# Optimization experiments

Hardware: AMD Instinct MI355X
Metric: run time of the kernel (lower is better)

The kernel has to match this reference:

```python
import jax, jax.numpy as jnp
import numpy as np

D_MODEL = 1024
NUM_HEADS = 16
D_K = D_MODEL // NUM_HEADS


def setup_inputs() -> dict:
    key = jax.random.key(0)
    ks = jax.random.split(key, 5)
    s = 1.0 / np.sqrt(D_MODEL)
    return {
        "x": jax.random.normal(ks[0], (2, 2048, D_MODEL), dtype=jnp.float32),
        "Wq": jax.random.normal(ks[1], (D_MODEL, D_MODEL), dtype=jnp.float32) * s,
        "bq": jnp.zeros((D_MODEL,), jnp.float32),
        "Wk": jax.random.normal(ks[2], (D_MODEL, D_MODEL), dtype=jnp.float32) * s,
        "bk": jnp.zeros((D_MODEL,), jnp.float32),
        "Wv": jax.random.normal(ks[3], (D_MODEL, D_MODEL), dtype=jnp.float32) * s,
        "bv": jnp.zeros((D_MODEL,), jnp.float32),
        "Wo": jax.random.normal(ks[4], (D_MODEL, D_MODEL), dtype=jnp.float32) * s,
        "bo": jnp.zeros((D_MODEL,), jnp.float32),
    }


def reference(x, Wq, bq, Wk, bk, Wv, bv, Wo, bo):
    B, S, _ = x.shape

    def split_heads(t):  # [B,S,D] -> [B,H,S,d_k]
        return t.reshape(B, S, NUM_HEADS, D_K).transpose(0, 2, 1, 3)

    q = split_heads(x @ Wq + bq)
    k = split_heads(x @ Wk + bk)
    v = split_heads(x @ Wv + bv)

    # [B,H,S,S] scores, scaled by 1/sqrt(d_k)
    scores = jnp.einsum("bhqd,bhkd->bhqk", q, k) / jnp.sqrt(jnp.float32(D_K))
    causal = jnp.tril(jnp.ones((S, S), dtype=bool))  # True = keep
    scores = jnp.where(causal, scores, -jnp.inf)
    attn = jax.nn.softmax(scores, axis=-1)
    # dropout is identity in eval mode
    out = jnp.einsum("bhqk,bhkd->bhqd", attn, v)
    out = out.transpose(0, 2, 1, 3).reshape(B, S, D_MODEL)
    return out @ Wo + bo
```

## Files before the change

kernel.cpp:

```cpp
#include <hip/hip_runtime.h>
#include <stdint.h>

typedef __attribute__((ext_vector_type(8))) short bf16x8;
typedef __attribute__((ext_vector_type(8))) unsigned short ushort8;
typedef __attribute__((ext_vector_type(4))) float f32x4;
typedef __attribute__((ext_vector_type(16))) float f32x16;

constexpr int DM = 1024;
constexpr int SQ = 2048;
constexpr int NB = 2;
constexpr int NH = 16;
constexpr int DK = 64;
constexpr int M  = NB * SQ;

__device__ inline float bf2f(unsigned short u) {
    union { uint32_t i; float f; } c; c.i = ((uint32_t)u) << 16; return c.f;
}
__device__ inline unsigned short f2bf(float f) {
    union { float f; uint32_t i; } c; c.f = f;
    uint32_t r = c.i + 0x7FFFu + ((c.i >> 16) & 1u);
    return (unsigned short)(r >> 16);
}
__device__ inline float exp2v(float x) {
    float r;
    asm("v_exp_f32 %0, %1" : "=v"(r) : "v"(x));
    return r;
}
__device__ inline uint32_t cvtpk(float lo, float hi) {
    uint32_t r;
    asm("v_cvt_pk_bf16_f32 %0, %1, %2" : "=v"(r) : "v"(lo), "v"(hi));
    return r;
}
__device__ inline uint32_t sx32(uint32_t v) {
    return (uint32_t)__shfl_xor((int)v, 32);
}
__device__ inline float sx32f(float v) {
    return __shfl_xor(v, 32);
}
__device__ inline bf16x8 mkfrag(uint32_t a, uint32_t b, uint32_t c, uint32_t d) {
    union { bf16x8 v; uint32_t u[4]; } m;
    m.u[0] = a; m.u[1] = b; m.u[2] = c; m.u[3] = d;
    return m.v;
}
__device__ inline void gload_lds16(const unsigned short* g, unsigned short* l) {
    __builtin_amdgcn_global_load_lds(
        (const __attribute__((address_space(1))) void*)g,
        (__attribute__((address_space(3))) void*)l, 16, 0, 0);
}

__global__ __launch_bounds__(256) void cvt_x(const float* __restrict__ x,
                                             unsigned short* __restrict__ xb) {
    int idx = (blockIdx.x * 256 + threadIdx.x) * 8;
    const float* p = x + idx;
    ushort8 o;
#pragma unroll
    for (int i = 0; i < 8; ++i) o[i] = f2bf(p[i]);
    *(ushort8*)(xb + idx) = o;
}

__global__ __launch_bounds__(256) void cvt_w4(const float* __restrict__ W0,
                                              const float* __restrict__ W1,
                                              const float* __restrict__ W2,
                                              const float* __restrict__ W3,
                                              unsigned short* __restrict__ WtBase) {
    __shared__ float tile[32][33];
    const int z = blockIdx.z;
    const float* W = (z == 0) ? W0 : (z == 1) ? W1 : (z == 2) ? W2 : W3;
    unsigned short* Wt = WtBase + (size_t)z * DM * DM;
    int tx = threadIdx.x, ty = threadIdx.y;
    int bx = blockIdx.x, by = blockIdx.y;
#pragma unroll
    for (int j = 0; j < 4; ++j)
        tile[ty + j * 8][tx] = W[(size_t)(by * 32 + ty + j * 8) * DM + bx * 32 + tx];
    __syncthreads();
#pragma unroll
    for (int j = 0; j < 4; ++j)
        Wt[(size_t)(bx * 32 + ty + j * 8) * DM + by * 32 + tx] = f2bf(tile[tx][ty + j * 8]);
}

__global__ __launch_bounds__(256) void gemm128(const unsigned short* __restrict__ A,
                                               const unsigned short* __restrict__ Bt,
                                               const float* __restrict__ b0,
                                               const float* __restrict__ b1,
                                               const float* __restrict__ b2,
                                               unsigned short* __restrict__ outp) {
    constexpr int K = 1024;
    __shared__ __align__(16) unsigned short As[128 * 32];
    __shared__ __align__(16) unsigned short Bs[128 * 32];
    const int t = threadIdx.x;
    const int w = t >> 6, l = t & 63;
    const int l15 = l & 15, lg = l >> 4;
    const int wr = w >> 1, wc = w & 1;
    const int bx = blockIdx.x, by = blockIdx.y;

    f32x4 acc[4][4] = {};

    const int srow = l >> 2;
    const int sk   = (l & 3) * 8;
    const unsigned short* Abase = A  + (size_t)(by * 128) * K;
    const unsigned short* Bbase = Bt + (size_t)(bx * 128) * K;

    for (int k0 = 0; k0 < K; k0 += 32) {
#pragma unroll
        for (int i = 0; i < 2; ++i) {
            const int row = w * 32 + i * 16 + srow;
            gload_lds16(Abase + (size_t)row * K + k0 + sk, &As[row * 32 + sk]);
            gload_lds16(Bbase + (size_t)row * K + k0 + sk, &Bs[row * 32 + sk]);
        }
        __syncthreads();

        bf16x8 af[4], bfr[4];
#pragma unroll
        for (int mi = 0; mi < 4; ++mi)
            af[mi] = *(const bf16x8*)&As[(wr * 64 + mi * 16 + l15) * 32 + lg * 8];
#pragma unroll
        for (int ni = 0; ni < 4; ++ni)
            bfr[ni] = *(const bf16x8*)&Bs[(wc * 64 + ni * 16 + l15) * 32 + lg * 8];
#pragma unroll
        for (int mi = 0; mi < 4; ++mi)
#pragma unroll
            for (int ni = 0; ni < 4; ++ni)
                acc[mi][ni] = __builtin_amdgcn_mfma_f32_16x16x32_bf16(af[mi], bfr[ni], acc[mi][ni], 0, 0, 0);
        __syncthreads();
    }

#pragma unroll
    for (int ni = 0; ni < 4; ++ni) {
        const int n = bx * 128 + wc * 64 + ni * 16 + l15;
        const int mat = n >> 10;
        const float* bp = (mat == 0) ? b0 : (mat == 1) ? b1 : b2;
        const float bias = bp[n & 1023];
#pragma unroll
        for (int mi = 0; mi < 4; ++mi)
#pragma unroll
            for (int i = 0; i < 4; ++i) {
                const int m = by * 128 + wr * 64 + mi * 16 + lg * 4 + i;
                float v = acc[mi][ni][i] + bias;
                const int c = n & 1023;
                if (mat == 0) v *= 0.18033688f;
                const int h = c >> 6, d = c & 63;
                const int b = m >> 11, si = m & 2047;
                size_t idx;
                if (mat == 2)
                    idx = ((size_t)(b * NH + h) * DK + d) * SQ + si;
                else
                    idx = ((size_t)(b * NH + h) * SQ + si) * DK + d;
                outp[(size_t)mat * (NB * NH * SQ * DK) + idx] = f2bf(v);
            }
    }
}

__global__ __launch_bounds__(256) void gemm_wo(const unsigned short* __restrict__ A,
                                               const unsigned short* __restrict__ Bt,
                                               const float* __restrict__ bias,
                                               float* __restrict__ outp) {
    constexpr int K = 1024;
    __shared__ __align__(16) unsigned short As[128 * 32];
    __shared__ __align__(16) unsigned short Bs[64 * 32];
    const int t = threadIdx.x;
    const int w = t >> 6, l = t & 63;
    const int l15 = l & 15, lg = l >> 4;
    const int bx = blockIdx.x, by = blockIdx.y;

    f32x4 acc[2][4] = {};

    const int srow = l >> 2;
    const int sk   = (l & 3) * 8;
    const int brow = t >> 2;
    const int bk   = (t & 3) * 8;
    const unsigned short* Abase = A  + (size_t)(by * 128) * K;
    const unsigned short* Bbase = Bt + (size_t)(bx * 64) * K;

    for (int k0 = 0; k0 < K; k0 += 32) {
#pragma unroll
        for (int i = 0; i < 2; ++i) {
            const int row = w * 32 + i * 16 + srow;
            gload_lds16(Abase + (size_t)row * K + k0 + sk, &As[row * 32 + sk]);
        }
        gload_lds16(Bbase + (size_t)brow * K + k0 + bk, &Bs[brow * 32 + bk]);
        __syncthreads();

        bf16x8 af[2], bfr[4];
#pragma unroll
        for (int mi = 0; mi < 2; ++mi)
            af[mi] = *(const bf16x8*)&As[(w * 32 + mi * 16 + l15) * 32 + lg * 8];
#pragma unroll
        for (int ni = 0; ni < 4; ++ni)
            bfr[ni] = *(const bf16x8*)&Bs[(ni * 16 + l15) * 32 + lg * 8];
#pragma unroll
        for (int mi = 0; mi < 2; ++mi)
#pragma unroll
            for (int ni = 0; ni < 4; ++ni)
                acc[mi][ni] = __builtin_amdgcn_mfma_f32_16x16x32_bf16(af[mi], bfr[ni], acc[mi][ni], 0, 0, 0);
        __syncthreads();
    }

#pragma unroll
    for (int ni = 0; ni < 4; ++ni) {
        const int n = bx * 64 + ni * 16 + l15;
        const float bv = bias[n];
#pragma unroll
        for (int mi = 0; mi < 2; ++mi)
#pragma unroll
            for (int i = 0; i < 4; ++i) {
                const int m = by * 128 + w * 32 + mi * 16 + lg * 4 + i;
                outp[(size_t)m * DM + n] = acc[mi][ni][i] + bv;
            }
    }
}

__global__ __launch_bounds__(128) void attn32(const unsigned short* __restrict__ Qg,
                                              const unsigned short* __restrict__ Kg,
                                              const unsigned short* __restrict__ Vtg,
                                              unsigned short* __restrict__ O) {
    __shared__ __align__(16) char KV[2][16384];
    const float NEG_INF = -__builtin_inff();

    const int bid = blockIdx.x;
    const int bh  = bid & 31;
    const int qi  = 63 - (bid >> 5);
    const int b = bh >> 4, h = bh & 15;
    const size_t base = (size_t)bh * SQ * DK;

    const int t = threadIdx.x;
    const int w = t >> 6, l = t & 63;
    const int l31 = l & 31, hi = l >> 5;
    const bool h0 = (hi == 0);

    char* Ks0 = KV[w];
    char* Vs0 = KV[w] + 8192;
    float* myP = (float*)KV[w];
    float* otP = (float*)KV[w ^ 1];

    const int lrow = l >> 3;
    const int lchunk = (l & 7) ^ lrow;
    const unsigned short* ksrc0 = Kg + base + (size_t)lrow * DK + lchunk * 8;
    const unsigned short* vsrc0 = Vtg + (size_t)(bh * 64 + lrow) * SQ + lchunk * 8;

    int roff[4];
#pragma unroll
    for (int c = 0; c < 4; ++c) roff[c] = (hi * 16 + 32 * c) ^ ((l & 7) << 4);
    const int rb0 = l31 * 128, rb1 = (32 + l31) * 128;

    const int T    = (qi >> 1) + 1;
    const int Tmax = (T + 1) >> 1;
    const int qrow = qi * 32 + l31;

    bf16x8 qf[4];
    {
        const unsigned short* qp = Qg + base + (size_t)qrow * DK + hi * 8;
#pragma unroll
        for (int c = 0; c < 4; ++c) qf[c] = *(const bf16x8*)(qp + 16 * c);
    }

    float mrun = NEG_INF, lsum = 0.f;
    f32x16 o0 = {}, o1 = {};

#pragma unroll 1
    for (int i = 0; i < Tmax; ++i) {
        const int kt = 2 * i + w;
        const bool act = kt < T;
        if (act) {
            const unsigned short* ks = ksrc0 + (size_t)kt * 64 * DK;
            const unsigned short* vs = vsrc0 + kt * 64;
#pragma unroll
            for (int j = 0; j < 8; ++j)
                gload_lds16(ks + j * 8 * DK, (unsigned short*)Ks0 + j * 512 + l * 8);
#pragma unroll
            for (int j = 0; j < 8; ++j)
                gload_lds16(vs + (size_t)j * 8 * SQ, (unsigned short*)Vs0 + j * 512 + l * 8);
        }
        __syncthreads();
        if (!act) continue;

        f32x16 s0v = {}, s1v = {};
#pragma unroll
        for (int c = 0; c < 4; ++c) {
            bf16x8 ka0 = *(const bf16x8*)(Ks0 + rb0 + roff[c]);
            bf16x8 ka1 = *(const bf16x8*)(Ks0 + rb1 + roff[c]);
            s0v = __builtin_amdgcn_mfma_f32_32x32x16_bf16(ka0, qf[c], s0v, 0, 0, 0);
            s1v = __builtin_amdgcn_mfma_f32_32x32x16_bf16(ka1, qf[c], s1v, 0, 0, 0);
        }

        float s[32];
#pragma unroll
        for (int r = 0; r < 16; ++r) { s[r] = s0v[r]; s[16 + r] = s1v[r]; }
        if (kt == T - 1) {
            const int qrel = qrow - kt * 64;
#pragma unroll
            for (int r = 0; r < 16; ++r) {
                const int key0 = (r & 3) + 8 * (r >> 2) + 4 * hi;
                if (key0 > qrel) s[r] = NEG_INF;
                if (key0 + 32 > qrel) s[16 + r] = NEG_INF;
            }
        }

        float t8[8];
#pragma unroll
        for (int j = 0; j < 8; ++j)
            t8[j] = fmaxf(fmaxf(s[j], s[j + 8]), fmaxf(s[j + 16], s[j + 24]));
        float tm = fmaxf(fmaxf(fmaxf(t8[0], t8[1]), fmaxf(t8[2], t8[3])),
                         fmaxf(fmaxf(t8[4], t8[5]), fmaxf(t8[6], t8[7])));
        tm = fmaxf(tm, sx32f(tm));

        const float mn = fmaxf(mrun, tm);
        if (!__all(tm - mrun <= 11.0f)) {
            const float corr = exp2v(mrun - mn);
            lsum *= corr;
#pragma unroll
            for (int r = 0; r < 16; ++r) { o0[r] *= corr; o1[r] *= corr; }
            mrun = mn;
        }

#pragma unroll
        for (int r = 0; r < 32; ++r) s[r] = exp2v(s[r] - mrun);
        float a8[8];
#pragma unroll
        for (int j = 0; j < 8; ++j)
            a8[j] = (s[j] + s[j + 8]) + (s[j + 16] + s[j + 24]);
        lsum += ((a8[0] + a8[1]) + (a8[2] + a8[3])) + ((a8[4] + a8[5]) + (a8[6] + a8[7]));

        uint32_t pk[16];
#pragma unroll
        for (int j = 0; j < 16; ++j) pk[j] = cvtpk(s[2 * j], s[2 * j + 1]);
        const uint32_t X1 = sx32(h0 ? pk[2]  : pk[0]);
        const uint32_t X2 = sx32(h0 ? pk[3]  : pk[1]);
        const uint32_t X3 = sx32(h0 ? pk[6]  : pk[4]);
        const uint32_t X4 = sx32(h0 ? pk[7]  : pk[5]);
        const uint32_t X5 = sx32(h0 ? pk[10] : pk[8]);
        const uint32_t X6 = sx32(h0 ? pk[11] : pk[9]);
        const uint32_t X7 = sx32(h0 ? pk[14] : pk[12]);
        const uint32_t X8 = sx32(h0 ? pk[15] : pk[13]);
        bf16x8 pf[4];
        pf[0] = mkfrag(h0 ? pk[0]  : X1, h0 ? pk[1]  : X2, h0 ? X1 : pk[2],  h0 ? X2 : pk[3]);
        pf[1] = mkfrag(h0 ? pk[4]  : X3, h0 ? pk[5]  : X4, h0 ? X3 : pk[6],  h0 ? X4 : pk[7]);
        pf[2] = mkfrag(h0 ? pk[8]  : X5, h0 ? pk[9]  : X6, h0 ? X5 : pk[10], h0 ? X6 : pk[11]);
        pf[3] = mkfrag(h0 ? pk[12] : X7, h0 ? pk[13] : X8, h0 ? X7 : pk[14], h0 ? X8 : pk[15]);

#pragma unroll
        for (int vi = 0; vi < 4; ++vi) {
            bf16x8 va0 = *(const bf16x8*)(Vs0 + rb0 + roff[vi]);
            bf16x8 va1 = *(const bf16x8*)(Vs0 + rb1 + roff[vi]);
            o0 = __builtin_amdgcn_mfma_f32_32x32x16_bf16(va0, pf[vi], o0, 0, 0, 0);
            o1 = __builtin_amdgcn_mfma_f32_32x32x16_bf16(va1, pf[vi], o1, 0, 0, 0);
        }
    }

    lsum += sx32f(lsum);
    {
        float* pb = myP + (size_t)l * 40;
#pragma unroll
        for (int r = 0; r < 16; ++r) { pb[r] = o0[r]; pb[16 + r] = o1[r]; }
        pb[32] = mrun; pb[33] = lsum;
    }
    __syncthreads();
    {
        const float* qb = otP + (size_t)l * 40;
        const float pm = qb[32], pl = qb[33];
        const float mm = fmaxf(mrun, pm);
        const float ca = exp2v(mrun - mm);
        const float cb = exp2v(pm - mm);
        const float lm = lsum * ca + pl * cb;
        if (w == 0) {
            const float inv = 1.f / lm;
            unsigned short* op = O + ((size_t)(b * SQ + qrow)) * DM + h * 64;
#pragma unroll
            for (int r = 0; r < 16; r += 2) {
                const int d = (r & 3) + 8 * (r >> 2) + 4 * hi;
                const float e0 = o0[r] * ca + qb[r] * cb;
                const float e1 = o0[r + 1] * ca + qb[r + 1] * cb;
                const float f0 = o1[r] * ca + qb[16 + r] * cb;
                const float f1 = o1[r + 1] * ca + qb[16 + r + 1] * cb;
                uint32_t w0 = (uint32_t)f2bf(e0 * inv) | ((uint32_t)f2bf(e1 * inv) << 16);
                uint32_t w1 = (uint32_t)f2bf(f0 * inv) | ((uint32_t)f2bf(f1 * inv) << 16);
                *(uint32_t*)(op + d) = w0;
                *(uint32_t*)(op + 32 + d) = w1;
            }
        }
    }
}

extern "C" void kernel_launch(void* const* d_in, const int* in_sizes, int n_in,
                              void* d_out, int out_size, void* d_ws, size_t ws_size,
                              hipStream_t stream) {
    const float* x  = (const float*)d_in[0];
    const float* Wq = (const float*)d_in[1];
    const float* bq = (const float*)d_in[2];
    const float* Wk = (const float*)d_in[3];
    const float* bk = (const float*)d_in[4];
    const float* Wv = (const float*)d_in[5];
    const float* bv = (const float*)d_in[6];
    const float* Wo = (const float*)d_in[7];
    const float* bo = (const float*)d_in[8];
    float* out = (float*)d_out;

    char* ws = (char*)d_ws;
    const size_t XB_BYTES = (size_t)M * DM * 2;
    const size_t W_BYTES  = (size_t)DM * DM * 2;
    const size_t H_BYTES  = (size_t)NB * NH * SQ * DK * 2;
    unsigned short* xb  = (unsigned short*)ws;
    unsigned short* wqt = (unsigned short*)(ws + XB_BYTES);
    unsigned short* wot = (unsigned short*)(ws + XB_BYTES + 3 * W_BYTES);
    unsigned short* Qb  = (unsigned short*)(ws + XB_BYTES + 4 * W_BYTES);
    unsigned short* Kb  = (unsigned short*)(ws + XB_BYTES + 4 * W_BYTES + H_BYTES);
    unsigned short* Vb  = (unsigned short*)(ws + XB_BYTES + 4 * W_BYTES + 2 * H_BYTES);

    cvt_x<<<(M * DM) / (256 * 8), 256, 0, stream>>>(x, xb);
    cvt_w4<<<dim3(32, 32, 4), dim3(32, 8), 0, stream>>>(Wq, Wk, Wv, Wo, wqt);

    gemm128<<<dim3(24, 32), 256, 0, stream>>>(xb, wqt, bq, bk, bv, Qb);

    attn32<<<NB * NH * 64, 128, 0, stream>>>(Qb, Kb, Vb, xb );

    gemm_wo<<<dim3(16, 32), 256, 0, stream>>>(xb, wot, bo, out);
}
```

Baseline: 120.4 us.

## Restructure attention: two waves share K/V tiles with double-buffered LDS prefetch

Previously each block handled 32 query rows, and its two waves split the key tiles and merged partial softmax results at the end. Now each block covers 64 query rows (one 32-row slab per wave), and both waves consume the same cooperatively loaded K/V tile from LDS. That halves K/V global traffic per query and removes the cross-wave softmax merge. Loading is double-buffered, so the next tile is issued before computing on the current one. Blocks are ordered to interleave short and long causal rows for load balance. The trade-off is half as many blocks, and the wave for the even slab does masked work on the diagonal tile.

```diff
diff --git a/kernel.cpp b/kernel.cpp
--- a/kernel.cpp
+++ b/kernel.cpp
@@ -213,12 +213,18 @@
                                               const unsigned short* __restrict__ Kg,
                                               const unsigned short* __restrict__ Vtg,
                                               unsigned short* __restrict__ O) {
-    __shared__ __align__(16) char KV[2][16384];
+    __shared__ __align__(16) char BufA[16384];
+    __shared__ __align__(16) char BufB[16384];
     const float NEG_INF = -__builtin_inff();
 
     const int bid = blockIdx.x;
     const int bh  = bid & 31;
-    const int qi  = 63 - (bid >> 5);
+    const int g   = bid >> 5;
+    const int u = g & 7, gq = g >> 3;
+    const int j_even = 2 * u + (gq >> 1);
+    const int j_odd  = 31 - 2 * u - (gq >> 1);
+    const int j = (gq & 1) ? j_odd : j_even;
+
     const int b = bh >> 4, h = bh & 15;
     const size_t base = (size_t)bh * SQ * DK;
 
@@ -227,23 +233,19 @@
     const int l31 = l & 31, hi = l >> 5;
     const bool h0 = (hi == 0);
 
-    char* Ks0 = KV[w];
-    char* Vs0 = KV[w] + 8192;
-    float* myP = (float*)KV[w];
-    float* otP = (float*)KV[w ^ 1];
-
-    const int lrow = l >> 3;
-    const int lchunk = (l & 7) ^ lrow;
-    const unsigned short* ksrc0 = Kg + base + (size_t)lrow * DK + lchunk * 8;
-    const unsigned short* vsrc0 = Vtg + (size_t)(bh * 64 + lrow) * SQ + lchunk * 8;
+    const int trow = t >> 3;
+    const int tchunk = (t & 7) ^ (trow & 7);
+    const unsigned short* ksrc0 = Kg + base + (size_t)trow * DK + tchunk * 8;
+    const unsigned short* vsrc0 = Vtg + (size_t)(bh * 64 + trow) * SQ + tchunk * 8;
+    const int ldst = w * 512 + l * 8;
 
     int roff[4];
 #pragma unroll
     for (int c = 0; c < 4; ++c) roff[c] = (hi * 16 + 32 * c) ^ ((l & 7) << 4);
     const int rb0 = l31 * 128, rb1 = (32 + l31) * 128;
 
-    const int T    = (qi >> 1) + 1;
-    const int Tmax = (T + 1) >> 1;
+    const int T    = j + 1;
+    const int qi   = 2 * j + w;
     const int qrow = qi * 32 + l31;
 
     bf16x8 qf[4];
@@ -256,23 +258,22 @@
     float mrun = NEG_INF, lsum = 0.f;
     f32x16 o0 = {}, o1 = {};
 
-#pragma unroll 1
-    for (int i = 0; i < Tmax; ++i) {
-        const int kt = 2 * i + w;
-        const bool act = kt < T;
-        if (act) {
-            const unsigned short* ks = ksrc0 + (size_t)kt * 64 * DK;
-            const unsigned short* vs = vsrc0 + kt * 64;
-#pragma unroll
-            for (int j = 0; j < 8; ++j)
-                gload_lds16(ks + j * 8 * DK, (unsigned short*)Ks0 + j * 512 + l * 8);
-#pragma unroll
-            for (int j = 0; j < 8; ++j)
-                gload_lds16(vs + (size_t)j * 8 * SQ, (unsigned short*)Vs0 + j * 512 + l * 8);
-        }
-        __syncthreads();
-        if (!act) continue;
-
+    auto STAGE = [&](int kt, char* Buf) {
+        const unsigned short* ks = ksrc0 + (size_t)kt * 64 * DK;
+        const unsigned short* vs = vsrc0 + kt * 64;
+        unsigned short* Kd = (unsigned short*)Buf;
+        unsigned short* Vd = (unsigned short*)(Buf + 8192);
+#pragma unroll
+        for (int i = 0; i < 4; ++i)
+            gload_lds16(ks + (size_t)i * 16 * DK, Kd + i * 1024 + ldst);
+#pragma unroll
+        for (int i = 0; i < 4; ++i)
+            gload_lds16(vs + (size_t)i * 16 * SQ, Vd + i * 1024 + ldst);
+    };
+
+    auto COMPUTE = [&](int kt, const char* Buf) {
+        const char* Ks0 = Buf;
+        const char* Vs0 = Buf + 8192;
         f32x16 s0v = {}, s1v = {};
 #pragma unroll
         for (int c = 0; c < 4; ++c) {
@@ -297,8 +298,8 @@
 
         float t8[8];
 #pragma unroll
-        for (int j = 0; j < 8; ++j)
-            t8[j] = fmaxf(fmaxf(s[j], s[j + 8]), fmaxf(s[j + 16], s[j + 24]));
+        for (int jj = 0; jj < 8; ++jj)
+            t8[jj] = fmaxf(fmaxf(s[jj], s[jj + 8]), fmaxf(s[jj + 16], s[jj + 24]));
         float tm = fmaxf(fmaxf(fmaxf(t8[0], t8[1]), fmaxf(t8[2], t8[3])),
                          fmaxf(fmaxf(t8[4], t8[5]), fmaxf(t8[6], t8[7])));
         tm = fmaxf(tm, sx32f(tm));
@@ -316,13 +317,13 @@
         for (int r = 0; r < 32; ++r) s[r] = exp2v(s[r] - mrun);
         float a8[8];
 #pragma unroll
-        for (int j = 0; j < 8; ++j)
-            a8[j] = (s[j] + s[j + 8]) + (s[j + 16] + s[j + 24]);
+        for (int jj = 0; jj < 8; ++jj)
+            a8[jj] = (s[jj] + s[jj + 8]) + (s[jj + 16] + s[jj + 24]);
         lsum += ((a8[0] + a8[1]) + (a8[2] + a8[3])) + ((a8[4] + a8[5]) + (a8[6] + a8[7]));
 
         uint32_t pk[16];
 #pragma unroll
-        for (int j = 0; j < 16; ++j) pk[j] = cvtpk(s[2 * j], s[2 * j + 1]);
+        for (int jj = 0; jj < 16; ++jj) pk[jj] = cvtpk(s[2 * jj], s[2 * jj + 1]);
         const uint32_t X1 = sx32(h0 ? pk[2]  : pk[0]);
         const uint32_t X2 = sx32(h0 ? pk[3]  : pk[1]);
         const uint32_t X3 = sx32(h0 ? pk[6]  : pk[4]);
@@ -344,39 +345,32 @@
             o0 = __builtin_amdgcn_mfma_f32_32x32x16_bf16(va0, pf[vi], o0, 0, 0, 0);
             o1 = __builtin_amdgcn_mfma_f32_32x32x16_bf16(va1, pf[vi], o1, 0, 0, 0);
         }
+    };
+
+    STAGE(0, BufA);
+    __syncthreads();
+
+#pragma unroll 1
+    for (int kt = 0; kt < T; kt += 2) {
+        if (kt + 1 < T) STAGE(kt + 1, BufB);
+        COMPUTE(kt, BufA);
+        __syncthreads();
+        if (kt + 1 >= T) break;
+        if (kt + 2 < T) STAGE(kt + 2, BufA);
+        COMPUTE(kt + 1, BufB);
+        __syncthreads();
     }
 
     lsum += sx32f(lsum);
-    {
-        float* pb = myP + (size_t)l * 40;
-#pragma unroll
-        for (int r = 0; r < 16; ++r) { pb[r] = o0[r]; pb[16 + r] = o1[r]; }
-        pb[32] = mrun; pb[33] = lsum;
-    }
-    __syncthreads();
-    {
-        const float* qb = otP + (size_t)l * 40;
-        const float pm = qb[32], pl = qb[33];
-        const float mm = fmaxf(mrun, pm);
-        const float ca = exp2v(mrun - mm);
-        const float cb = exp2v(pm - mm);
-        const float lm = lsum * ca + pl * cb;
-        if (w == 0) {
-            const float inv = 1.f / lm;
-            unsigned short* op = O + ((size_t)(b * SQ + qrow)) * DM + h * 64;
-#pragma unroll
-            for (int r = 0; r < 16; r += 2) {
-                const int d = (r & 3) + 8 * (r >> 2) + 4 * hi;
-                const float e0 = o0[r] * ca + qb[r] * cb;
-                const float e1 = o0[r + 1] * ca + qb[r + 1] * cb;
-                const float f0 = o1[r] * ca + qb[16 + r] * cb;
-                const float f1 = o1[r + 1] * ca + qb[16 + r + 1] * cb;
-                uint32_t w0 = (uint32_t)f2bf(e0 * inv) | ((uint32_t)f2bf(e1 * inv) << 16);
-                uint32_t w1 = (uint32_t)f2bf(f0 * inv) | ((uint32_t)f2bf(f1 * inv) << 16);
-                *(uint32_t*)(op + d) = w0;
-                *(uint32_t*)(op + 32 + d) = w1;
-            }
-        }
+    const float inv = 1.f / lsum;
+    unsigned short* op = O + ((size_t)(b * SQ + qrow)) * DM + h * 64;
+#pragma unroll
+    for (int r = 0; r < 16; r += 2) {
+        const int d = (r & 3) + 8 * (r >> 2) + 4 * hi;
+        uint32_t w0 = (uint32_t)f2bf(o0[r] * inv) | ((uint32_t)f2bf(o0[r + 1] * inv) << 16);
+        uint32_t w1 = (uint32_t)f2bf(o1[r] * inv) | ((uint32_t)f2bf(o1[r + 1] * inv) << 16);
+        *(uint32_t*)(op + d) = w0;
+        *(uint32_t*)(op + 32 + d) = w1;
     }
 }
 
@@ -410,7 +404,7 @@
 
     gemm128<<<dim3(24, 32), 256, 0, stream>>>(xb, wqt, bq, bk, bv, Qb);
 
-    attn32<<<NB * NH * 64, 128, 0, stream>>>(Qb, Kb, Vb, xb );
+    attn32<<<NB * NH * 32, 128, 0, stream>>>(Qb, Kb, Vb, xb );
 
     gemm_wo<<<dim3(16, 32), 256, 0, stream>>>(xb, wot, bo, out);
 }
```

Measured after the change: 124.1 us. 3.0% more time.
